# Optimization experiments

Measured on AMD Instinct MI355X. Metric: run time of the kernel, lower is better.

The kernel has to match this reference:

```python
import jax, jax.numpy as jnp
import numpy as np

B, N, D, E = 64, 512, 256, 524288
VOCAB, NTYPES = 50000, 8
NUM_NODES = B * N


def setup_inputs() -> dict:
    key = jax.random.key(0)
    ks = jax.random.split(key, 20)
    p = lambda k, shape: jax.random.normal(k, shape, jnp.float32) * 0.05
    return {
        'x_tokens': jax.random.randint(ks[0], (NUM_NODES,), 0, VOCAB),
        'word_type': jax.random.randint(ks[1], (NUM_NODES,), 0, NTYPES),
        'edge_index': jax.random.randint(ks[2], (2, E), 0, NUM_NODES),
        'edge_attr': jax.random.uniform(ks[3], (E,), jnp.float32),
        'mask_pad': jnp.ones((B, N, 1), jnp.float32),
        'mask_score': jnp.zeros((B, N), jnp.float32),
        'emb_table': p(ks[4], (VOCAB, D)),
        'wt_table': p(ks[5], (NTYPES, D)),
        'W_w': p(ks[6], (D, D)), 'b_w': jnp.zeros((D,), jnp.float32),
        'W_g1': p(ks[7], (D, D)), 'b_g1': jnp.zeros((D,), jnp.float32),
        'W_g2': p(ks[8], (D, D)), 'b_g2': jnp.zeros((D,), jnp.float32),
        'W_p1': p(ks[9], (D, D)), 'b_p1': jnp.zeros((D,), jnp.float32),
        'W_p2': p(ks[10], (D, 1)),
        'Wih_x': p(ks[11], (4 * D, D)), 'Whh_x': p(ks[12], (4 * D, D)),
        'bih_x': jnp.zeros((4 * D,), jnp.float32), 'bhh_x': jnp.zeros((4 * D,), jnp.float32),
        'Wih_g': p(ks[13], (4 * D, D)), 'Whh_g': p(ks[14], (4 * D, D)),
        'bih_g': jnp.zeros((4 * D,), jnp.float32), 'bhh_g': jnp.zeros((4 * D,), jnp.float32),
    }


def _lstm_cell(x, h, c, Wih, Whh, bih, bhh):
    g = x @ Wih.T + h @ Whh.T + (bih + bhh)
    i, f, gg, o = jnp.split(g, 4, axis=-1)  # torch gate order: i, f, g, o
    c = jax.nn.sigmoid(f) * c + jax.nn.sigmoid(i) * jnp.tanh(gg)
    h = jax.nn.sigmoid(o) * jnp.tanh(c)
    return h, c


def _lstm_last(x0, x1, Wih, Whh, bih, bhh):
    # batch_first LSTM over seq-len-2 input; return last hidden output
    z = jnp.zeros_like(x0)
    h, c = _lstm_cell(x0, z, z, Wih, Whh, bih, bhh)
    h, _ = _lstm_cell(x1, h, c, Wih, Whh, bih, bhh)
    return h


def _gcn(x, src, dst, ew, W, b):
    # PyG GCNConv with edge_weight: add self-loops (w=1), symmetric norm
    deg = jax.ops.segment_sum(ew, dst, NUM_NODES) + 1.0
    dinv = jax.lax.rsqrt(deg)
    norm = dinv[src] * ew * dinv[dst]  # [E]
    xw = x @ W                         # [NUM_NODES, D]
    out = jax.ops.segment_sum(norm[:, None] * xw[src], dst, NUM_NODES)
    out = out + (dinv * dinv)[:, None] * xw  # self-loop contribution
    return out + b


def _pool(x2d, W_p1, b_p1, W_p2, mask_score):
    x3 = x2d.reshape(B, N, D)
    h = jnp.tanh(x3 @ W_p1 + b_p1)
    score = (h @ W_p2)[..., 0] + mask_score  # [B, N]
    alpha = jax.nn.softmax(score, axis=-1)
    return jnp.sum(alpha[..., None] * x3, axis=1)  # [B, D]


def reference(x_tokens, word_type, edge_index, edge_attr, mask_pad, mask_score,
              emb_table, wt_table, W_w, b_w, W_g1, b_g1, W_g2, b_g2,
              W_p1, b_p1, W_p2, Wih_x, Whh_x, bih_x, bhh_x,
              Wih_g, Whh_g, bih_g, bhh_g):
    src, dst = edge_index[0], edge_index[1]
    x = emb_table[x_tokens] + wt_table[word_type]  # use_wordtype == True
    x = x @ W_w + b_w
    x1_mid = _gcn(x, src, dst, edge_attr, W_g1, b_g1)
    x1 = _lstm_last(x, x1_mid, Wih_x, Whh_x, bih_x, bhh_x)
    g1 = _pool(x1, W_p1, b_p1, W_p2, mask_score)
    x2_mid = _gcn(x1, src, dst, edge_attr, W_g2, b_g2)
    x2 = _lstm_last(x1, x2_mid, Wih_x, Whh_x, bih_x, bhh_x)
    g2 = _pool(x2, W_p1, b_p1, W_p2, mask_score)
    graph_out = _lstm_last(g1, g2, Wih_g, Whh_g, bih_g, bhh_g)  # [B, D]
    x_out = jnp.tanh(x2).reshape(B, N, D) * mask_pad
    return x_out, graph_out
```

## Files before the change

kernel.cpp:

```cpp
#include <hip/hip_runtime.h>
#include <hip/hip_bf16.h>
#include <math.h>

#define NODES 32768
#define DD 256
#define NE 524288
#define BATCH 64
#define SEQ 512

__device__ __forceinline__ float sigf(float x) { return 1.0f / (1.0f + expf(-x)); }

__global__ __launch_bounds__(256) void embed_kernel(const int* __restrict__ tok,
                                                    const int* __restrict__ wty,
                                                    const float* __restrict__ emb,
                                                    const float* __restrict__ wt,
                                                    float* __restrict__ x) {
    int i = blockIdx.x;
    int d = threadIdx.x;
    x[i * DD + d] = emb[tok[i] * DD + d] + wt[wty[i] * DD + d];
}

template <bool BIAS, bool TANH>
__global__ __launch_bounds__(256) void gemm_nn(const float* __restrict__ A,
                                               const float* __restrict__ B,
                                               const float* __restrict__ bias,
                                               float* __restrict__ C, int M) {
    __shared__ float As[16][68];
    __shared__ float Bs[16][68];
    const int m0 = blockIdx.x * 64;
    const int n0 = blockIdx.y * 64;
    const int t = threadIdx.x;
    const int ty = t >> 4, tx = t & 15;
    const int lm = t >> 2;
    const int lk4 = (t & 3) * 4;
    const int bkk = t >> 4;
    const int bn4 = (t & 15) * 4;

    float acc[4][4] = {};
    for (int k0 = 0; k0 < 256; k0 += 16) {
        float4 av = *(const float4*)&A[(m0 + lm) * 256 + k0 + lk4];
        float4 bv = *(const float4*)&B[(k0 + bkk) * 256 + n0 + bn4];
        __syncthreads();
        As[lk4 + 0][lm] = av.x; As[lk4 + 1][lm] = av.y;
        As[lk4 + 2][lm] = av.z; As[lk4 + 3][lm] = av.w;
        *(float4*)&Bs[bkk][bn4] = bv;
        __syncthreads();
#pragma unroll
        for (int kk = 0; kk < 16; ++kk) {
            float4 a = *(const float4*)&As[kk][ty * 4];
            float4 b = *(const float4*)&Bs[kk][tx * 4];
            float av4[4] = {a.x, a.y, a.z, a.w};
            float bv4[4] = {b.x, b.y, b.z, b.w};
#pragma unroll
            for (int i = 0; i < 4; ++i)
#pragma unroll
                for (int j = 0; j < 4; ++j)
                    acc[i][j] = fmaf(av4[i], bv4[j], acc[i][j]);
        }
    }
#pragma unroll
    for (int i = 0; i < 4; ++i) {
        int r = m0 + ty * 4 + i;
        float o[4];
#pragma unroll
        for (int j = 0; j < 4; ++j) {
            float v = acc[i][j];
            if (BIAS) v += bias[n0 + tx * 4 + j];
            if (TANH) v = tanhf(v);
            o[j] = v;
        }
        *(float4*)&C[r * 256 + n0 + tx * 4] = make_float4(o[0], o[1], o[2], o[3]);
    }
}

template <bool FIRST>
__global__ __launch_bounds__(256) void lstm_gemm(const float* __restrict__ X,
                                                 const float* __restrict__ H,
                                                 const float* __restrict__ Wih,
                                                 const float* __restrict__ Whh,
                                                 const float* __restrict__ bih,
                                                 const float* __restrict__ bhh,
                                                 const float* __restrict__ c_in,
                                                 float* __restrict__ c_out,
                                                 float* __restrict__ h_out, int M) {
    __shared__ float As[16][68];
    __shared__ float Bs[4][16][68];
    const int m0 = blockIdx.x * 64;
    const int n0 = blockIdx.y * 64;
    const int t = threadIdx.x;
    const int ty = t >> 4, tx = t & 15;
    const int lm = t >> 2;
    const int lk4 = (t & 3) * 4;

    float acc[4][4][4] = {};
    const int npass = FIRST ? 1 : 2;
    for (int pass = 0; pass < npass; ++pass) {
        const float* Ain = pass ? H : X;
        const float* W = pass ? Whh : Wih;
        for (int k0 = 0; k0 < 256; k0 += 16) {
            float4 av = *(const float4*)&Ain[(m0 + lm) * 256 + k0 + lk4];
            float4 w0 = *(const float4*)&W[(0 * 256 + n0 + lm) * 256 + k0 + lk4];
            float4 w1 = *(const float4*)&W[(1 * 256 + n0 + lm) * 256 + k0 + lk4];
            float4 w2 = *(const float4*)&W[(2 * 256 + n0 + lm) * 256 + k0 + lk4];
            float4 w3 = *(const float4*)&W[(3 * 256 + n0 + lm) * 256 + k0 + lk4];
            __syncthreads();
            As[lk4 + 0][lm] = av.x; As[lk4 + 1][lm] = av.y;
            As[lk4 + 2][lm] = av.z; As[lk4 + 3][lm] = av.w;
            Bs[0][lk4 + 0][lm] = w0.x; Bs[0][lk4 + 1][lm] = w0.y;
            Bs[0][lk4 + 2][lm] = w0.z; Bs[0][lk4 + 3][lm] = w0.w;
            Bs[1][lk4 + 0][lm] = w1.x; Bs[1][lk4 + 1][lm] = w1.y;
            Bs[1][lk4 + 2][lm] = w1.z; Bs[1][lk4 + 3][lm] = w1.w;
            Bs[2][lk4 + 0][lm] = w2.x; Bs[2][lk4 + 1][lm] = w2.y;
            Bs[2][lk4 + 2][lm] = w2.z; Bs[2][lk4 + 3][lm] = w2.w;
            Bs[3][lk4 + 0][lm] = w3.x; Bs[3][lk4 + 1][lm] = w3.y;
            Bs[3][lk4 + 2][lm] = w3.z; Bs[3][lk4 + 3][lm] = w3.w;
            __syncthreads();
#pragma unroll
            for (int kk = 0; kk < 16; ++kk) {
                float4 a = *(const float4*)&As[kk][ty * 4];
                float av4[4] = {a.x, a.y, a.z, a.w};
#pragma unroll
                for (int g = 0; g < 4; ++g) {
                    float4 b = *(const float4*)&Bs[g][kk][tx * 4];
                    float bv4[4] = {b.x, b.y, b.z, b.w};
#pragma unroll
                    for (int i = 0; i < 4; ++i)
#pragma unroll
                        for (int j = 0; j < 4; ++j)
                            acc[g][i][j] = fmaf(av4[i], bv4[j], acc[g][i][j]);
                }
            }
        }
    }
#pragma unroll
    for (int i = 0; i < 4; ++i) {
        int r = m0 + ty * 4 + i;
#pragma unroll
        for (int j = 0; j < 4; ++j) {
            int dcol = n0 + tx * 4 + j;
            float gi = acc[0][i][j] + bih[dcol] + bhh[dcol];
            float gf = acc[1][i][j] + bih[256 + dcol] + bhh[256 + dcol];
            float gg = acc[2][i][j] + bih[512 + dcol] + bhh[512 + dcol];
            float go = acc[3][i][j] + bih[768 + dcol] + bhh[768 + dcol];
            float cprev = FIRST ? 0.0f : c_in[r * 256 + dcol];
            float cv = sigf(gf) * cprev + sigf(gi) * tanhf(gg);
            float hv = sigf(go) * tanhf(cv);
            c_out[r * 256 + dcol] = cv;
            h_out[r * 256 + dcol] = hv;
        }
    }
}

__global__ __launch_bounds__(256) void csr_init(int* __restrict__ counts, float* __restrict__ deg) {
    int i = blockIdx.x * 256 + threadIdx.x;
    counts[i] = 0;
    deg[i] = 1.0f;
}
__global__ __launch_bounds__(256) void csr_hist(const int* __restrict__ dst,
                                                const float* __restrict__ ew,
                                                int* __restrict__ counts,
                                                float* __restrict__ deg) {
    int e = blockIdx.x * 256 + threadIdx.x;
    int d = dst[e];
    atomicAdd(&counts[d], 1);
    atomicAdd(&deg[d], ew[e]);
}
__global__ __launch_bounds__(256) void csr_dinv(float* __restrict__ deg) {
    int i = blockIdx.x * 256 + threadIdx.x;
    deg[i] = 1.0f / sqrtf(deg[i]);
}
__global__ __launch_bounds__(256) void csr_scan(const int* __restrict__ counts,
                                                int* __restrict__ offs,
                                                int* __restrict__ cursor) {
    __shared__ int part[256];
    int t = threadIdx.x;
    int base = t * 128;
    int s = 0;
    for (int k = 0; k < 128; ++k) s += counts[base + k];
    part[t] = s;
    __syncthreads();
    for (int off = 1; off < 256; off <<= 1) {
        int v = part[t];
        int add = (t >= off) ? part[t - off] : 0;
        __syncthreads();
        part[t] = v + add;
        __syncthreads();
    }
    int run = part[t] - s;
    for (int k = 0; k < 128; ++k) {
        int c = counts[base + k];
        offs[base + k] = run;
        cursor[base + k] = run;
        run += c;
    }
    if (t == 255) offs[NODES] = run;
}
__global__ __launch_bounds__(256) void csr_fill(const int* __restrict__ src,
                                                const int* __restrict__ dst,
                                                const float* __restrict__ ew,
                                                const float* __restrict__ dinv,
                                                int* __restrict__ cursor,
                                                int* __restrict__ es,
                                                float* __restrict__ en) {
    int e = blockIdx.x * 256 + threadIdx.x;
    int s = src[e], d = dst[e];
    int pos = atomicAdd(&cursor[d], 1);
    es[pos] = s;
    en[pos] = dinv[s] * ew[e] * dinv[d];
}

__global__ __launch_bounds__(256) void gcn_gather(const float* __restrict__ x,
                                                  const int* __restrict__ offs,
                                                  const int* __restrict__ es,
                                                  const float* __restrict__ en,
                                                  const float* __restrict__ dinv,
                                                  float* __restrict__ agg) {
    int i = blockIdx.x;
    int d = threadIdx.x;
    float di = dinv[i];
    float acc = di * di * x[i * DD + d];
    int a = offs[i], b = offs[i + 1];
    for (int j = a; j < b; ++j) {
        int s = es[j];
        float w = en[j];
        acc += w * x[s * DD + d];
    }
    agg[i * DD + d] = acc;
}

__global__ __launch_bounds__(256) void score_kernel(const float* __restrict__ htmp,
                                                    const float* __restrict__ Wp2,
                                                    const float* __restrict__ mask_score,
                                                    float* __restrict__ score) {
    int m = blockIdx.x * 4 + (threadIdx.x >> 6);
    int l = threadIdx.x & 63;
    float4 h = *(const float4*)&htmp[m * DD + l * 4];
    float4 w = *(const float4*)&Wp2[l * 4];
    float d = h.x * w.x + h.y * w.y + h.z * w.z + h.w * w.w;
#pragma unroll
    for (int off = 32; off; off >>= 1) d += __shfl_down(d, off);
    if (l == 0) score[m] = d + mask_score[m];
}

__global__ __launch_bounds__(256) void pool_kernel(const float* __restrict__ x,
                                                   const float* __restrict__ score,
                                                   float* __restrict__ gout) {
    int b = blockIdx.x;
    int t = threadIdx.x;
    __shared__ float sal[512];
    __shared__ float wred[4];
    __shared__ float sbc[2];
    int lane = t & 63, wv = t >> 6;
    float s0 = score[b * SEQ + t];
    float s1 = score[b * SEQ + 256 + t];
    float m = fmaxf(s0, s1);
#pragma unroll
    for (int off = 32; off; off >>= 1) m = fmaxf(m, __shfl_down(m, off));
    if (lane == 0) wred[wv] = m;
    __syncthreads();
    if (t == 0) sbc[0] = fmaxf(fmaxf(wred[0], wred[1]), fmaxf(wred[2], wred[3]));
    __syncthreads();
    float mx = sbc[0];
    float e0 = expf(s0 - mx), e1 = expf(s1 - mx);
    sal[t] = e0;
    sal[t + 256] = e1;
    float sm = e0 + e1;
#pragma unroll
    for (int off = 32; off; off >>= 1) sm += __shfl_down(sm, off);
    __syncthreads();
    if (lane == 0) wred[wv] = sm;
    __syncthreads();
    if (t == 0) sbc[1] = wred[0] + wred[1] + wred[2] + wred[3];
    __syncthreads();
    float inv = 1.0f / sbc[1];
    float accv = 0.0f;
    const float* xb = x + (size_t)b * SEQ * DD + t;
    for (int n = 0; n < SEQ; ++n) accv += sal[n] * xb[n * DD];
    gout[b * DD + t] = accv * inv;
}

__global__ __launch_bounds__(256) void final_kernel(const float* __restrict__ x2,
                                                    const float* __restrict__ mask_pad,
                                                    float* __restrict__ out) {
    int i = blockIdx.x;
    int d = threadIdx.x;
    out[i * DD + d] = tanhf(x2[i * DD + d]) * mask_pad[i];
}

extern "C" void kernel_launch(void* const* d_in, const int* in_sizes, int n_in,
                              void* d_out, int out_size, void* d_ws, size_t ws_size,
                              hipStream_t stream) {
    const int* x_tokens = (const int*)d_in[0];
    const int* word_type = (const int*)d_in[1];
    const int* edge_src = (const int*)d_in[2];
    const int* edge_dst = edge_src + NE;
    const float* edge_attr = (const float*)d_in[3];
    const float* mask_pad = (const float*)d_in[4];
    const float* mask_score = (const float*)d_in[5];
    const float* emb = (const float*)d_in[6];
    const float* wt = (const float*)d_in[7];
    const float* W_w = (const float*)d_in[8];
    const float* b_w = (const float*)d_in[9];
    const float* W_g1 = (const float*)d_in[10];
    const float* b_g1 = (const float*)d_in[11];
    const float* W_g2 = (const float*)d_in[12];
    const float* b_g2 = (const float*)d_in[13];
    const float* W_p1 = (const float*)d_in[14];
    const float* b_p1 = (const float*)d_in[15];
    const float* W_p2 = (const float*)d_in[16];
    const float* Wih_x = (const float*)d_in[17];
    const float* Whh_x = (const float*)d_in[18];
    const float* bih_x = (const float*)d_in[19];
    const float* bhh_x = (const float*)d_in[20];
    const float* Wih_g = (const float*)d_in[21];
    const float* Whh_g = (const float*)d_in[22];
    const float* bih_g = (const float*)d_in[23];
    const float* bhh_g = (const float*)d_in[24];

    float* out = (float*)d_out;
    char* ws = (char*)d_ws;

    int* counts = (int*)ws;
    int* cursor = counts + NODES;
    int* offs = cursor + NODES;
    float* dinv = (float*)(offs + NODES + 64);
    float* score = dinv + NODES;
    float* g1 = score + NODES;
    float* g2 = g1 + BATCH * DD;
    float* hg = g2 + BATCH * DD;
    float* cg = hg + BATCH * DD;
    int* es = (int*)(cg + BATCH * DD);
    float* en = (float*)(es + NE);
    const size_t NDf = (size_t)NODES * DD;
    float* base = (float*)(ws + (6u << 20));
    float* B1 = base;
    float* B2 = base + NDf;
    float* B3 = base + 2 * NDf;
    float* OUTB = out;

    dim3 blk(256);
    dim3 gemmGrid(NODES / 64, 4);

    csr_init<<<NODES / 256, blk, 0, stream>>>(counts, dinv);
    csr_hist<<<NE / 256, blk, 0, stream>>>(edge_dst, edge_attr, counts, dinv);
    csr_dinv<<<NODES / 256, blk, 0, stream>>>(dinv);
    csr_scan<<<1, blk, 0, stream>>>(counts, offs, cursor);
    csr_fill<<<NE / 256, blk, 0, stream>>>(edge_src, edge_dst, edge_attr, dinv, cursor, es, en);

    embed_kernel<<<NODES, blk, 0, stream>>>(x_tokens, word_type, emb, wt, B1);
    gemm_nn<true, false><<<gemmGrid, blk, 0, stream>>>(B1, W_w, b_w, B2, NODES);
    gcn_gather<<<NODES, blk, 0, stream>>>(B2, offs, es, en, dinv, B1);
    gemm_nn<true, false><<<gemmGrid, blk, 0, stream>>>(B1, W_g1, b_g1, B3, NODES);
    lstm_gemm<true><<<gemmGrid, blk, 0, stream>>>(B2, nullptr, Wih_x, Whh_x, bih_x, bhh_x,
                                                  nullptr, OUTB, B1, NODES);
    lstm_gemm<false><<<gemmGrid, blk, 0, stream>>>(B3, B1, Wih_x, Whh_x, bih_x, bhh_x,
                                                   OUTB, OUTB, B2, NODES);
    gemm_nn<true, true><<<gemmGrid, blk, 0, stream>>>(B2, W_p1, b_p1, B3, NODES);
    score_kernel<<<NODES / 4, blk, 0, stream>>>(B3, W_p2, mask_score, score);
    pool_kernel<<<BATCH, blk, 0, stream>>>(B2, score, g1);
    gcn_gather<<<NODES, blk, 0, stream>>>(B2, offs, es, en, dinv, B1);
    gemm_nn<true, false><<<gemmGrid, blk, 0, stream>>>(B1, W_g2, b_g2, B3, NODES);
    lstm_gemm<true><<<gemmGrid, blk, 0, stream>>>(B2, nullptr, Wih_x, Whh_x, bih_x, bhh_x,
                                                  nullptr, OUTB, B1, NODES);
    lstm_gemm<false><<<gemmGrid, blk, 0, stream>>>(B3, B1, Wih_x, Whh_x, bih_x, bhh_x,
                                                   OUTB, OUTB, B2, NODES);
    gemm_nn<true, true><<<gemmGrid, blk, 0, stream>>>(B2, W_p1, b_p1, B3, NODES);
    score_kernel<<<NODES / 4, blk, 0, stream>>>(B3, W_p2, mask_score, score);
    pool_kernel<<<BATCH, blk, 0, stream>>>(B2, score, g2);
    lstm_gemm<true><<<dim3(1, 4), blk, 0, stream>>>(g1, nullptr, Wih_g, Whh_g, bih_g, bhh_g,
                                                    nullptr, cg, hg, BATCH);
    lstm_gemm<false><<<dim3(1, 4), blk, 0, stream>>>(g2, hg, Wih_g, Whh_g, bih_g, bhh_g,
                                                     cg, cg, out + NODES * DD, BATCH);
    final_kernel<<<NODES, blk, 0, stream>>>(B2, mask_pad, out);
}
```

Measured before the change: 2.245 ms.

## Use split-bf16 MFMA GEMMs with hi/lo activation storage for node-level matmuls

```diff
diff --git a/kernel.cpp b/kernel.cpp
--- a/kernel.cpp
+++ b/kernel.cpp
@@ -8,68 +8,171 @@
 #define BATCH 64
 #define SEQ 512
 
+typedef __attribute__((ext_vector_type(8))) short short8v;
+typedef __attribute__((ext_vector_type(4))) float f32x4;
+typedef unsigned short u16;
+
 __device__ __forceinline__ float sigf(float x) { return 1.0f / (1.0f + expf(-x)); }
-
-__global__ __launch_bounds__(256) void embed_kernel(const int* __restrict__ tok,
-                                                    const int* __restrict__ wty,
-                                                    const float* __restrict__ emb,
-                                                    const float* __restrict__ wt,
-                                                    float* __restrict__ x) {
-    int i = blockIdx.x;
-    int d = threadIdx.x;
-    x[i * DD + d] = emb[tok[i] * DD + d] + wt[wty[i] * DD + d];
-}
-
-template <bool BIAS, bool TANH>
-__global__ __launch_bounds__(256) void gemm_nn(const float* __restrict__ A,
-                                               const float* __restrict__ B,
-                                               const float* __restrict__ bias,
-                                               float* __restrict__ C, int M) {
-    __shared__ float As[16][68];
-    __shared__ float Bs[16][68];
-    const int m0 = blockIdx.x * 64;
-    const int n0 = blockIdx.y * 64;
-    const int t = threadIdx.x;
-    const int ty = t >> 4, tx = t & 15;
-    const int lm = t >> 2;
-    const int lk4 = (t & 3) * 4;
-    const int bkk = t >> 4;
-    const int bn4 = (t & 15) * 4;
-
-    float acc[4][4] = {};
-    for (int k0 = 0; k0 < 256; k0 += 16) {
-        float4 av = *(const float4*)&A[(m0 + lm) * 256 + k0 + lk4];
-        float4 bv = *(const float4*)&B[(k0 + bkk) * 256 + n0 + bn4];
-        __syncthreads();
-        As[lk4 + 0][lm] = av.x; As[lk4 + 1][lm] = av.y;
-        As[lk4 + 2][lm] = av.z; As[lk4 + 3][lm] = av.w;
-        *(float4*)&Bs[bkk][bn4] = bv;
-        __syncthreads();
-#pragma unroll
-        for (int kk = 0; kk < 16; ++kk) {
-            float4 a = *(const float4*)&As[kk][ty * 4];
-            float4 b = *(const float4*)&Bs[kk][tx * 4];
-            float av4[4] = {a.x, a.y, a.z, a.w};
-            float bv4[4] = {b.x, b.y, b.z, b.w};
-#pragma unroll
-            for (int i = 0; i < 4; ++i)
-#pragma unroll
-                for (int j = 0; j < 4; ++j)
-                    acc[i][j] = fmaf(av4[i], bv4[j], acc[i][j]);
+__device__ __forceinline__ float bfu(u16 u) {
+    unsigned int x = ((unsigned int)u) << 16;
+    float f;
+    __builtin_memcpy(&f, &x, 4);
+    return f;
+}
+__device__ __forceinline__ u16 f2b(float f) {
+    __hip_bfloat16 h = __float2bfloat16(f);
+    u16 u;
+    __builtin_memcpy(&u, &h, 2);
+    return u;
+}
+__device__ __forceinline__ void split_store(float v, u16* __restrict__ hi, u16* __restrict__ lo, int idx) {
+    u16 h = f2b(v);
+    hi[idx] = h;
+    lo[idx] = f2b(v - bfu(h));
+}
+
+__global__ __launch_bounds__(256) void wsplitT(const float* __restrict__ W,
+                                               u16* __restrict__ h, u16* __restrict__ l) {
+    int n = blockIdx.x, k = threadIdx.x;
+    split_store(W[k * 256 + n], h, l, n * 256 + k);
+}
+__global__ __launch_bounds__(256) void wsplit(const float* __restrict__ W,
+                                              u16* __restrict__ h, u16* __restrict__ l) {
+    int i = blockIdx.x * 256 + threadIdx.x;
+    split_store(W[i], h, l, i);
+}
+
+__global__ __launch_bounds__(256) void embed_split(const int* __restrict__ tok,
+                                                   const int* __restrict__ wty,
+                                                   const float* __restrict__ emb,
+                                                   const float* __restrict__ wt,
+                                                   u16* __restrict__ xh, u16* __restrict__ xl) {
+    int i = blockIdx.x, d = threadIdx.x;
+    float v = emb[tok[i] * DD + d] + wt[wty[i] * DD + d];
+    split_store(v, xh, xl, i * DD + d);
+}
+
+template <bool TANH>
+__global__ __launch_bounds__(256) void mfma_gemm(const u16* __restrict__ Ah, const u16* __restrict__ Al,
+                                                 const u16* __restrict__ Bh, const u16* __restrict__ Bl,
+                                                 const float* __restrict__ bias,
+                                                 u16* __restrict__ Chi, u16* __restrict__ Clo) {
+    const int l = threadIdx.x & 63, w = threadIdx.x >> 6;
+    const int m0 = blockIdx.x * 64, n0 = w * 64;
+    const int lr = l & 15, lk = (l >> 4) * 8;
+    f32x4 acc[4][4];
+#pragma unroll
+    for (int mi = 0; mi < 4; ++mi)
+#pragma unroll
+        for (int ni = 0; ni < 4; ++ni) acc[mi][ni] = (f32x4){0.f, 0.f, 0.f, 0.f};
+
+    const u16* APtr[3] = {Ah, Ah, Al};
+    const u16* BPtr[3] = {Bh, Bl, Bh};
+    for (int term = 0; term < 3; ++term) {
+        const u16* A = APtr[term];
+        const u16* B = BPtr[term];
+#pragma unroll
+        for (int kb = 0; kb < 8; ++kb) {
+            int ka = kb * 32 + lk;
+            short8v a[4], b[4];
+#pragma unroll
+            for (int mi = 0; mi < 4; ++mi)
+                a[mi] = *(const short8v*)&A[(m0 + mi * 16 + lr) * 256 + ka];
+#pragma unroll
+            for (int ni = 0; ni < 4; ++ni)
+                b[ni] = *(const short8v*)&B[(n0 + ni * 16 + lr) * 256 + ka];
+#pragma unroll
+            for (int mi = 0; mi < 4; ++mi)
+#pragma unroll
+                for (int ni = 0; ni < 4; ++ni)
+                    acc[mi][ni] = __builtin_amdgcn_mfma_f32_16x16x32_bf16(a[mi], b[ni], acc[mi][ni], 0, 0, 0);
         }
     }
 #pragma unroll
-    for (int i = 0; i < 4; ++i) {
-        int r = m0 + ty * 4 + i;
-        float o[4];
-#pragma unroll
-        for (int j = 0; j < 4; ++j) {
-            float v = acc[i][j];
-            if (BIAS) v += bias[n0 + tx * 4 + j];
-            if (TANH) v = tanhf(v);
-            o[j] = v;
+    for (int mi = 0; mi < 4; ++mi)
+#pragma unroll
+        for (int ni = 0; ni < 4; ++ni) {
+            int col = n0 + ni * 16 + lr;
+            float bs = bias[col];
+#pragma unroll
+            for (int r = 0; r < 4; ++r) {
+                int row = m0 + mi * 16 + (l >> 4) * 4 + r;
+                float v = acc[mi][ni][r] + bs;
+                if (TANH) v = tanhf(v);
+                split_store(v, Chi, Clo, row * 256 + col);
+            }
         }
-        *(float4*)&C[r * 256 + n0 + tx * 4] = make_float4(o[0], o[1], o[2], o[3]);
+}
+
+template <bool FIRST>
+__global__ __launch_bounds__(256) void mfma_lstm(const u16* __restrict__ Xh, const u16* __restrict__ Xl,
+                                                 const u16* __restrict__ Hh, const u16* __restrict__ Hl,
+                                                 const u16* __restrict__ Wih_h, const u16* __restrict__ Wih_l,
+                                                 const u16* __restrict__ Whh_h, const u16* __restrict__ Whh_l,
+                                                 const float* __restrict__ bih, const float* __restrict__ bhh,
+                                                 const float* __restrict__ c_in, float* __restrict__ c_out,
+                                                 u16* __restrict__ Ohi, u16* __restrict__ Olo) {
+    __shared__ float lds[4][64][65];
+    const int l = threadIdx.x & 63, g = threadIdx.x >> 6;
+    const int m0 = blockIdx.x * 64, d0 = blockIdx.y * 64;
+    const int lr = l & 15, lk = (l >> 4) * 8;
+    f32x4 acc[4][4];
+#pragma unroll
+    for (int mi = 0; mi < 4; ++mi)
+#pragma unroll
+        for (int ni = 0; ni < 4; ++ni) acc[mi][ni] = (f32x4){0.f, 0.f, 0.f, 0.f};
+
+    const int npass = FIRST ? 1 : 2;
+    for (int pass = 0; pass < npass; ++pass) {
+        const u16* Ih = pass ? Hh : Xh;
+        const u16* Il = pass ? Hl : Xl;
+        const u16* Wh = pass ? Whh_h : Wih_h;
+        const u16* Wl = pass ? Whh_l : Wih_l;
+        const u16* APtr[3] = {Ih, Ih, Il};
+        const u16* BPtr[3] = {Wh, Wl, Wh};
+        for (int term = 0; term < 3; ++term) {
+            const u16* A = APtr[term];
+            const u16* B = BPtr[term];
+#pragma unroll
+            for (int kb = 0; kb < 8; ++kb) {
+                int ka = kb * 32 + lk;
+                short8v a[4], b[4];
+#pragma unroll
+                for (int mi = 0; mi < 4; ++mi)
+                    a[mi] = *(const short8v*)&A[(m0 + mi * 16 + lr) * 256 + ka];
+#pragma unroll
+                for (int ni = 0; ni < 4; ++ni)
+                    b[ni] = *(const short8v*)&B[(g * 256 + d0 + ni * 16 + lr) * 256 + ka];
+#pragma unroll
+                for (int mi = 0; mi < 4; ++mi)
+#pragma unroll
+                    for (int ni = 0; ni < 4; ++ni)
+                        acc[mi][ni] = __builtin_amdgcn_mfma_f32_16x16x32_bf16(a[mi], b[ni], acc[mi][ni], 0, 0, 0);
+            }
+        }
+    }
+#pragma unroll
+    for (int mi = 0; mi < 4; ++mi)
+#pragma unroll
+        for (int ni = 0; ni < 4; ++ni)
+#pragma unroll
+            for (int r = 0; r < 4; ++r)
+                lds[g][mi * 16 + (l >> 4) * 4 + r][ni * 16 + lr] = acc[mi][ni][r];
+    __syncthreads();
+#pragma unroll 4
+    for (int rep = 0; rep < 16; ++rep) {
+        int idx = rep * 256 + threadIdx.x;
+        int ml = idx >> 6, dl = idx & 63;
+        int row = m0 + ml, d = d0 + dl;
+        float gi = lds[0][ml][dl] + bih[d] + bhh[d];
+        float gf = lds[1][ml][dl] + bih[256 + d] + bhh[256 + d];
+        float gg = lds[2][ml][dl] + bih[512 + d] + bhh[512 + d];
+        float go = lds[3][ml][dl] + bih[768 + d] + bhh[768 + d];
+        float cprev = FIRST ? 0.0f : c_in[row * 256 + d];
+        float cv = sigf(gf) * cprev + sigf(gi) * tanhf(gg);
+        float hv = sigf(go) * tanhf(cv);
+        c_out[row * 256 + d] = cv;
+        split_store(hv, Ohi, Olo, row * 256 + d);
     }
 }
 
@@ -91,7 +194,6 @@
     const int ty = t >> 4, tx = t & 15;
     const int lm = t >> 2;
     const int lk4 = (t & 3) * 4;
-
     float acc[4][4][4] = {};
     const int npass = FIRST ? 1 : 2;
     for (int pass = 0; pass < npass; ++pass) {
@@ -120,14 +222,14 @@
                 float4 a = *(const float4*)&As[kk][ty * 4];
                 float av4[4] = {a.x, a.y, a.z, a.w};
 #pragma unroll
-                for (int g = 0; g < 4; ++g) {
-                    float4 b = *(const float4*)&Bs[g][kk][tx * 4];
+                for (int gg = 0; gg < 4; ++gg) {
+                    float4 b = *(const float4*)&Bs[gg][kk][tx * 4];
                     float bv4[4] = {b.x, b.y, b.z, b.w};
 #pragma unroll
                     for (int i = 0; i < 4; ++i)
 #pragma unroll
                         for (int j = 0; j < 4; ++j)
-                            acc[g][i][j] = fmaf(av4[i], bv4[j], acc[g][i][j]);
+                            acc[gg][i][j] = fmaf(av4[i], bv4[j], acc[gg][i][j]);
                 }
             }
         }
@@ -209,40 +311,41 @@
     en[pos] = dinv[s] * ew[e] * dinv[d];
 }
 
-__global__ __launch_bounds__(256) void gcn_gather(const float* __restrict__ x,
+__global__ __launch_bounds__(256) void gcn_gather(const u16* __restrict__ xh, const u16* __restrict__ xl,
                                                   const int* __restrict__ offs,
                                                   const int* __restrict__ es,
                                                   const float* __restrict__ en,
                                                   const float* __restrict__ dinv,
-                                                  float* __restrict__ agg) {
-    int i = blockIdx.x;
-    int d = threadIdx.x;
+                                                  u16* __restrict__ oh, u16* __restrict__ ol) {
+    int i = blockIdx.x, d = threadIdx.x;
     float di = dinv[i];
-    float acc = di * di * x[i * DD + d];
+    float acc = di * di * (bfu(xh[i * DD + d]) + bfu(xl[i * DD + d]));
     int a = offs[i], b = offs[i + 1];
     for (int j = a; j < b; ++j) {
         int s = es[j];
         float w = en[j];
-        acc += w * x[s * DD + d];
-    }
-    agg[i * DD + d] = acc;
-}
-
-__global__ __launch_bounds__(256) void score_kernel(const float* __restrict__ htmp,
+        acc += w * (bfu(xh[s * DD + d]) + bfu(xl[s * DD + d]));
+    }
+    split_store(acc, oh, ol, i * DD + d);
+}
+
+__global__ __launch_bounds__(256) void score_kernel(const u16* __restrict__ hh, const u16* __restrict__ hl,
                                                     const float* __restrict__ Wp2,
                                                     const float* __restrict__ mask_score,
                                                     float* __restrict__ score) {
     int m = blockIdx.x * 4 + (threadIdx.x >> 6);
     int l = threadIdx.x & 63;
-    float4 h = *(const float4*)&htmp[m * DD + l * 4];
+    ushort4 a = *(const ushort4*)&hh[m * DD + l * 4];
+    ushort4 b = *(const ushort4*)&hl[m * DD + l * 4];
     float4 w = *(const float4*)&Wp2[l * 4];
-    float d = h.x * w.x + h.y * w.y + h.z * w.z + h.w * w.w;
+    float d = (bfu(a.x) + bfu(b.x)) * w.x + (bfu(a.y) + bfu(b.y)) * w.y +
+              (bfu(a.z) + bfu(b.z)) * w.z + (bfu(a.w) + bfu(b.w)) * w.w;
 #pragma unroll
     for (int off = 32; off; off >>= 1) d += __shfl_down(d, off);
     if (l == 0) score[m] = d + mask_score[m];
 }
 
-__global__ __launch_bounds__(256) void pool_kernel(const float* __restrict__ x,
+__global__ __launch_bounds__(256) void pool_kernel(const u16* __restrict__ xh, const u16* __restrict__ xl,
                                                    const float* __restrict__ score,
                                                    float* __restrict__ gout) {
     int b = blockIdx.x;
@@ -274,17 +377,18 @@
     __syncthreads();
     float inv = 1.0f / sbc[1];
     float accv = 0.0f;
-    const float* xb = x + (size_t)b * SEQ * DD + t;
-    for (int n = 0; n < SEQ; ++n) accv += sal[n] * xb[n * DD];
+    size_t base = (size_t)b * SEQ * DD + t;
+    for (int n = 0; n < SEQ; ++n)
+        accv += sal[n] * (bfu(xh[base + (size_t)n * DD]) + bfu(xl[base + (size_t)n * DD]));
     gout[b * DD + t] = accv * inv;
 }
 
-__global__ __launch_bounds__(256) void final_kernel(const float* __restrict__ x2,
+__global__ __launch_bounds__(256) void final_kernel(const u16* __restrict__ xh, const u16* __restrict__ xl,
                                                     const float* __restrict__ mask_pad,
                                                     float* __restrict__ out) {
-    int i = blockIdx.x;
-    int d = threadIdx.x;
-    out[i * DD + d] = tanhf(x2[i * DD + d]) * mask_pad[i];
+    int i = blockIdx.x, d = threadIdx.x;
+    float v = bfu(xh[i * DD + d]) + bfu(xl[i * DD + d]);
+    out[i * DD + d] = tanhf(v) * mask_pad[i];
 }
 
 extern "C" void kernel_launch(void* const* d_in, const int* in_sizes, int n_in,
@@ -331,15 +435,24 @@
     float* cg = hg + BATCH * DD;
     int* es = (int*)(cg + BATCH * DD);
     float* en = (float*)(es + NE);
+    u16* wsm = (u16*)(en + NE);
+    u16* wwTh = wsm;               u16* wwTl = wwTh + 65536;
+    u16* wg1h = wwTl + 65536;      u16* wg1l = wg1h + 65536;
+    u16* wg2h = wg1l + 65536;      u16* wg2l = wg2h + 65536;
+    u16* wp1h = wg2l + 65536;      u16* wp1l = wp1h + 65536;
+    u16* wihh = wp1l + 65536;      u16* wihl = wihh + 262144;
+    u16* whhh = wihl + 262144;     u16* whhl = whhh + 262144;
+
     const size_t NDf = (size_t)NODES * DD;
-    float* base = (float*)(ws + (6u << 20));
-    float* B1 = base;
-    float* B2 = base + NDf;
-    float* B3 = base + 2 * NDf;
+    u16* base = (u16*)(ws + (8u << 20));
+    u16* S1h = base;               u16* S1l = S1h + NDf;
+    u16* S2h = S1l + NDf;          u16* S2l = S2h + NDf;
+    u16* S3h = S2l + NDf;          u16* S3l = S3h + NDf;
     float* OUTB = out;
 
     dim3 blk(256);
-    dim3 gemmGrid(NODES / 64, 4);
+    dim3 gemmGrid(NODES / 64);
+    dim3 lstmGrid(NODES / 64, 4);
 
     csr_init<<<NODES / 256, blk, 0, stream>>>(counts, dinv);
     csr_hist<<<NE / 256, blk, 0, stream>>>(edge_dst, edge_attr, counts, dinv);
@@ -347,29 +460,36 @@
     csr_scan<<<1, blk, 0, stream>>>(counts, offs, cursor);
     csr_fill<<<NE / 256, blk, 0, stream>>>(edge_src, edge_dst, edge_attr, dinv, cursor, es, en);
 
-    embed_kernel<<<NODES, blk, 0, stream>>>(x_tokens, word_type, emb, wt, B1);
-    gemm_nn<true, false><<<gemmGrid, blk, 0, stream>>>(B1, W_w, b_w, B2, NODES);
-    gcn_gather<<<NODES, blk, 0, stream>>>(B2, offs, es, en, dinv, B1);
-    gemm_nn<true, false><<<gemmGrid, blk, 0, stream>>>(B1, W_g1, b_g1, B3, NODES);
-    lstm_gemm<true><<<gemmGrid, blk, 0, stream>>>(B2, nullptr, Wih_x, Whh_x, bih_x, bhh_x,
-                                                  nullptr, OUTB, B1, NODES);
-    lstm_gemm<false><<<gemmGrid, blk, 0, stream>>>(B3, B1, Wih_x, Whh_x, bih_x, bhh_x,
-                                                   OUTB, OUTB, B2, NODES);
-    gemm_nn<true, true><<<gemmGrid, blk, 0, stream>>>(B2, W_p1, b_p1, B3, NODES);
-    score_kernel<<<NODES / 4, blk, 0, stream>>>(B3, W_p2, mask_score, score);
-    pool_kernel<<<BATCH, blk, 0, stream>>>(B2, score, g1);
-    gcn_gather<<<NODES, blk, 0, stream>>>(B2, offs, es, en, dinv, B1);
-    gemm_nn<true, false><<<gemmGrid, blk, 0, stream>>>(B1, W_g2, b_g2, B3, NODES);
-    lstm_gemm<true><<<gemmGrid, blk, 0, stream>>>(B2, nullptr, Wih_x, Whh_x, bih_x, bhh_x,
-                                                  nullptr, OUTB, B1, NODES);
-    lstm_gemm<false><<<gemmGrid, blk, 0, stream>>>(B3, B1, Wih_x, Whh_x, bih_x, bhh_x,
-                                                   OUTB, OUTB, B2, NODES);
-    gemm_nn<true, true><<<gemmGrid, blk, 0, stream>>>(B2, W_p1, b_p1, B3, NODES);
-    score_kernel<<<NODES / 4, blk, 0, stream>>>(B3, W_p2, mask_score, score);
-    pool_kernel<<<BATCH, blk, 0, stream>>>(B2, score, g2);
+    wsplitT<<<256, blk, 0, stream>>>(W_w, wwTh, wwTl);
+    wsplitT<<<256, blk, 0, stream>>>(W_g1, wg1h, wg1l);
+    wsplitT<<<256, blk, 0, stream>>>(W_g2, wg2h, wg2l);
+    wsplitT<<<256, blk, 0, stream>>>(W_p1, wp1h, wp1l);
+    wsplit<<<1024, blk, 0, stream>>>(Wih_x, wihh, wihl);
+    wsplit<<<1024, blk, 0, stream>>>(Whh_x, whhh, whhl);
+
+    embed_split<<<NODES, blk, 0, stream>>>(x_tokens, word_type, emb, wt, S1h, S1l);
+    mfma_gemm<false><<<gemmGrid, blk, 0, stream>>>(S1h, S1l, wwTh, wwTl, b_w, S2h, S2l);
+    gcn_gather<<<NODES, blk, 0, stream>>>(S2h, S2l, offs, es, en, dinv, S1h, S1l);
+    mfma_gemm<false><<<gemmGrid, blk, 0, stream>>>(S1h, S1l, wg1h, wg1l, b_g1, S3h, S3l);
+    mfma_lstm<true><<<lstmGrid, blk, 0, stream>>>(S2h, S2l, nullptr, nullptr, wihh, wihl, whhh, whhl,
+                                                  bih_x, bhh_x, nullptr, OUTB, S1h, S1l);
+    mfma_lstm<false><<<lstmGrid, blk, 0, stream>>>(S3h, S3l, S1h, S1l, wihh, wihl, whhh, whhl,
+                                                   bih_x, bhh_x, OUTB, OUTB, S2h, S2l);
+    mfma_gemm<true><<<gemmGrid, blk, 0, stream>>>(S2h, S2l, wp1h, wp1l, b_p1, S3h, S3l);
+    score_kernel<<<NODES / 4, blk, 0, stream>>>(S3h, S3l, W_p2, mask_score, score);
+    pool_kernel<<<BATCH, blk, 0, stream>>>(S2h, S2l, score, g1);
+    gcn_gather<<<NODES, blk, 0, stream>>>(S2h, S2l, offs, es, en, dinv, S1h, S1l);
+    mfma_gemm<false><<<gemmGrid, blk, 0, stream>>>(S1h, S1l, wg2h, wg2l, b_g2, S3h, S3l);
+    mfma_lstm<true><<<lstmGrid, blk, 0, stream>>>(S2h, S2l, nullptr, nullptr, wihh, wihl, whhh, whhl,
+                                                  bih_x, bhh_x, nullptr, OUTB, S1h, S1l);
+    mfma_lstm<false><<<lstmGrid, blk, 0, stream>>>(S3h, S3l, S1h, S1l, wihh, wihl, whhh, whhl,
+                                                   bih_x, bhh_x, OUTB, OUTB, S2h, S2l);
+    mfma_gemm<true><<<gemmGrid, blk, 0, stream>>>(S2h, S2l, wp1h, wp1l, b_p1, S3h, S3l);
+    score_kernel<<<NODES / 4, blk, 0, stream>>>(S3h, S3l, W_p2, mask_score, score);
+    pool_kernel<<<BATCH, blk, 0, stream>>>(S2h, S2l, score, g2);
     lstm_gemm<true><<<dim3(1, 4), blk, 0, stream>>>(g1, nullptr, Wih_g, Whh_g, bih_g, bhh_g,
                                                     nullptr, cg, hg, BATCH);
     lstm_gemm<false><<<dim3(1, 4), blk, 0, stream>>>(g2, hg, Wih_g, Whh_g, bih_g, bhh_g,
                                                      cg, cg, out + NODES * DD, BATCH);
-    final_kernel<<<NODES, blk, 0, stream>>>(B2, mask_pad, out);
-}
+    final_kernel<<<NODES, blk, 0, stream>>>(S2h, S2l, mask_pad, out);
+}
```

New measurement: 2.118 ms. 5.7% less time.
